# Performance work log

Measured on AMD Instinct MI355X. Metric: run time of the kernel, lower is better.

## Reference

```python
import jax, jax.numpy as jnp
import numpy as np

N, D, H, C = 50000, 128, 4, 16  # nodes, in_dim, heads, out per head
E, ED = 800000, 64              # edges, edge feature dim
NEG_SLOPE = 0.2


def setup_inputs() -> dict:
    key = jax.random.key(0)
    ks = jax.random.split(key, 10)
    x = jax.random.normal(ks[0], (N, D), dtype=jnp.float32)
    edge_index = jax.random.randint(ks[1], (2, E), 0, N, dtype=jnp.int64)
    edge_attr = jax.random.normal(ks[2], (E, ED), dtype=jnp.float32)
    s = 0.1
    W = jax.random.normal(ks[3], (H * C, D), dtype=jnp.float32) * s       # lin (no bias)
    W_edge = jax.random.normal(ks[4], (H * C, ED), dtype=jnp.float32) * s  # lin_edge (no bias)
    att_src = jax.random.normal(ks[5], (H, C), dtype=jnp.float32) * s
    att_dst = jax.random.normal(ks[6], (H, C), dtype=jnp.float32) * s
    att_edge = jax.random.normal(ks[7], (H, C), dtype=jnp.float32) * s
    bias = jnp.zeros((H * C,), dtype=jnp.float32)
    return dict(x=x, edge_index=edge_index, edge_attr=edge_attr, W=W,
                W_edge=W_edge, att_src=att_src, att_dst=att_dst,
                att_edge=att_edge, bias=bias)


def reference(x, edge_index, edge_attr, W, W_edge, att_src, att_dst, att_edge, bias):
    n = x.shape[0]
    src0, dst0 = edge_index[0], edge_index[1]

    # PyG GATConv default: add self-loops, self-loop edge_attr = per-dst mean of incoming edge_attr
    ones = jnp.ones((src0.shape[0],), dtype=edge_attr.dtype)
    cnt = jax.ops.segment_sum(ones, dst0, num_segments=n)                # [N]
    loop_attr = jax.ops.segment_sum(edge_attr, dst0, num_segments=n)
    loop_attr = loop_attr / jnp.maximum(cnt, 1.0)[:, None]               # [N, ED]
    ar = jnp.arange(n, dtype=src0.dtype)
    src = jnp.concatenate([src0, ar])
    dst = jnp.concatenate([dst0, ar])
    ea = jnp.concatenate([edge_attr, loop_attr], axis=0)                 # [E+N, ED]

    xh = (x @ W.T).reshape(n, H, C)                                      # [N, H, C]
    a_src = jnp.einsum('nhc,hc->nh', xh, att_src)                        # [N, H]
    a_dst = jnp.einsum('nhc,hc->nh', xh, att_dst)
    eh = (ea @ W_edge.T).reshape(-1, H, C)                               # [E+N, H, C]
    a_edge = jnp.einsum('ehc,hc->eh', eh, att_edge)                      # [E+N, H]

    alpha = a_src[src] + a_dst[dst] + a_edge                             # [E+N, H]
    alpha = jax.nn.leaky_relu(alpha, NEG_SLOPE)

    # softmax over edges grouped by destination node (PyG softmax)
    amax = jax.ops.segment_max(alpha, dst, num_segments=n)               # [N, H]
    alpha = jnp.exp(alpha - amax[dst])
    denom = jax.ops.segment_sum(alpha, dst, num_segments=n)
    alpha = alpha / (denom[dst] + 1e-16)

    # message = x_j * alpha, scatter-add to destination
    out = jax.ops.segment_sum(xh[src] * alpha[:, :, None], dst, num_segments=n)  # [N,H,C]
    return out.reshape(n, H * C) + bias
```

## Files before the change

kernel.cpp:

```cpp
#include <hip/hip_runtime.h>
#include <math.h>

#define N_NODES 50000
#define DIM     128
#define NHEAD   4
#define NCH     16
#define HC      64
#define NE      800000
#define EDIM    64
#define NEG     0.2f
#define MAXE    64

__device__ __forceinline__ float lrelu(float v) { return v > 0.f ? v : NEG * v; }

__global__ void k1_vedge(const float* __restrict__ W_edge, const float* __restrict__ att_edge,
                         float* __restrict__ v_edge) {
    int t = threadIdx.x;
    int h = t >> 6, d = t & 63;
    float acc = 0.f;
    #pragma unroll
    for (int c = 0; c < NCH; ++c)
        acc = fmaf(att_edge[h * NCH + c], W_edge[(h * NCH + c) * EDIM + d], acc);
    v_edge[h * 64 + d] = acc;
}

__global__ __launch_bounds__(256) void k2_xh(const float* __restrict__ x, const float* __restrict__ W,
                                             const float* __restrict__ att_src, const float* __restrict__ att_dst,
                                             float* __restrict__ xh, float* __restrict__ a_src,
                                             float* __restrict__ a_dst) {
    __shared__ float Wt[128 * 68];
    int t = threadIdx.x;
    for (int idx = t; idx < 64 * 128; idx += 256) {
        int col = idx >> 7, k = idx & 127;
        Wt[k * 68 + col] = W[idx];
    }
    __syncthreads();

    int h  = t & 3;
    int rp = t >> 2;
    int row0 = blockIdx.x * 128 + rp * 2;
    int r0 = min(row0, N_NODES - 1);
    int r1 = min(row0 + 1, N_NODES - 1);
    const float4* x0 = (const float4*)(x + (size_t)r0 * DIM);
    const float4* x1 = (const float4*)(x + (size_t)r1 * DIM);

    float acc0[16], acc1[16];
    #pragma unroll
    for (int c = 0; c < 16; ++c) { acc0[c] = 0.f; acc1[c] = 0.f; }

    for (int k4 = 0; k4 < 32; ++k4) {
        float4 xa = x0[k4];
        float4 xb = x1[k4];
        #pragma unroll
        for (int kk = 0; kk < 4; ++kk) {
            float va = (&xa.x)[kk];
            float vb = (&xb.x)[kk];
            const float* wr = &Wt[(k4 * 4 + kk) * 68 + h * 16];
            #pragma unroll
            for (int j = 0; j < 4; ++j) {
                float4 w = *(const float4*)(wr + 4 * j);
                acc0[4 * j + 0] = fmaf(va, w.x, acc0[4 * j + 0]);
                acc0[4 * j + 1] = fmaf(va, w.y, acc0[4 * j + 1]);
                acc0[4 * j + 2] = fmaf(va, w.z, acc0[4 * j + 2]);
                acc0[4 * j + 3] = fmaf(va, w.w, acc0[4 * j + 3]);
                acc1[4 * j + 0] = fmaf(vb, w.x, acc1[4 * j + 0]);
                acc1[4 * j + 1] = fmaf(vb, w.y, acc1[4 * j + 1]);
                acc1[4 * j + 2] = fmaf(vb, w.z, acc1[4 * j + 2]);
                acc1[4 * j + 3] = fmaf(vb, w.w, acc1[4 * j + 3]);
            }
        }
    }

    if (row0 < N_NODES) {
        float4* o = (float4*)(xh + (size_t)row0 * HC + h * 16);
        o[0] = make_float4(acc0[0], acc0[1], acc0[2], acc0[3]);
        o[1] = make_float4(acc0[4], acc0[5], acc0[6], acc0[7]);
        o[2] = make_float4(acc0[8], acc0[9], acc0[10], acc0[11]);
        o[3] = make_float4(acc0[12], acc0[13], acc0[14], acc0[15]);
        float ss = 0.f, sd = 0.f;
        #pragma unroll
        for (int c = 0; c < 16; ++c) {
            ss = fmaf(acc0[c], att_src[h * 16 + c], ss);
            sd = fmaf(acc0[c], att_dst[h * 16 + c], sd);
        }
        a_src[row0 * 4 + h] = ss;
        a_dst[row0 * 4 + h] = sd;
    }
    if (row0 + 1 < N_NODES) {
        float4* o = (float4*)(xh + (size_t)(row0 + 1) * HC + h * 16);
        o[0] = make_float4(acc1[0], acc1[1], acc1[2], acc1[3]);
        o[1] = make_float4(acc1[4], acc1[5], acc1[6], acc1[7]);
        o[2] = make_float4(acc1[8], acc1[9], acc1[10], acc1[11]);
        o[3] = make_float4(acc1[12], acc1[13], acc1[14], acc1[15]);
        float ss = 0.f, sd = 0.f;
        #pragma unroll
        for (int c = 0; c < 16; ++c) {
            ss = fmaf(acc1[c], att_src[h * 16 + c], ss);
            sd = fmaf(acc1[c], att_dst[h * 16 + c], sd);
        }
        a_src[(row0 + 1) * 4 + h] = ss;
        a_dst[(row0 + 1) * 4 + h] = sd;
    }
}

__global__ __launch_bounds__(256) void ka_deg(const int* __restrict__ ei, int* __restrict__ deg) {
    int e = blockIdx.x * 256 + threadIdx.x;
    if (e >= NE) return;
    atomicAdd(deg + ei[NE + e], 1);
}

__global__ void k4a_scan(const int* __restrict__ deg, int* __restrict__ tmp, int* __restrict__ bsums) {
    int t = threadIdx.x;
    int i = blockIdx.x * 256 + t;
    int v = (i < N_NODES) ? deg[i] : 0;
    int lane = t & 63, w = t >> 6;
    int xv = v;
    #pragma unroll
    for (int o = 1; o < 64; o <<= 1) {
        int y = __shfl_up(xv, o);
        if (lane >= o) xv += y;
    }
    __shared__ int wtot[4];
    if (lane == 63) wtot[w] = xv;
    __syncthreads();
    int add = 0;
    #pragma unroll
    for (int j = 0; j < 4; ++j)
        if (j < w) add += wtot[j];
    xv += add;
    if (i < N_NODES) tmp[i] = xv;
    if (t == 255) bsums[blockIdx.x] = xv;
}

__global__ void k4b_scan(int* __restrict__ bsums, int nb) {
    int t = threadIdx.x;
    int v = (t < nb) ? bsums[t] : 0;
    int lane = t & 63, w = t >> 6;
    int xv = v;
    #pragma unroll
    for (int o = 1; o < 64; o <<= 1) {
        int y = __shfl_up(xv, o);
        if (lane >= o) xv += y;
    }
    __shared__ int wtot[4];
    if (lane == 63) wtot[w] = xv;
    __syncthreads();
    int add = 0;
    #pragma unroll
    for (int j = 0; j < 4; ++j)
        if (j < w) add += wtot[j];
    xv += add;
    if (t < nb) bsums[t] = xv - v;
}

__global__ void k4c_finish(const int* __restrict__ tmp, const int* __restrict__ bsums,
                           const int* __restrict__ deg, int* __restrict__ rowptr,
                           int* __restrict__ cursor) {
    int i = blockIdx.x * 256 + threadIdx.x;
    if (i >= N_NODES) return;
    int incl = tmp[i] + bsums[i >> 8];
    rowptr[i + 1] = incl;
    cursor[i] = incl - deg[i];
    if (i == 0) rowptr[0] = 0;
}

__global__ __launch_bounds__(256) void kp_csr(const float* __restrict__ edge_attr,
                                              const int* __restrict__ ei,
                                              const float* __restrict__ v_edge,
                                              int* __restrict__ cursor,
                                              int* __restrict__ csr_src,
                                              float* __restrict__ csr_p) {
    int lane = threadIdx.x & 63;
    int q = lane & 15;
    float4 w0 = *(const float4*)(v_edge + 0 * 64 + q * 4);
    float4 w1 = *(const float4*)(v_edge + 1 * 64 + q * 4);
    float4 w2 = *(const float4*)(v_edge + 2 * 64 + q * 4);
    float4 w3 = *(const float4*)(v_edge + 3 * 64 + q * 4);

    int wave   = (blockIdx.x * 256 + threadIdx.x) >> 6;
    int nwaves = gridDim.x * 4;
    for (int g = wave; g < NE / 4; g += nwaves) {
        float4 v = *(const float4*)(edge_attr + (size_t)g * 256 + lane * 4);
        float p0 = fmaf(v.x, w0.x, fmaf(v.y, w0.y, fmaf(v.z, w0.z, v.w * w0.w)));
        float p1 = fmaf(v.x, w1.x, fmaf(v.y, w1.y, fmaf(v.z, w1.z, v.w * w1.w)));
        float p2 = fmaf(v.x, w2.x, fmaf(v.y, w2.y, fmaf(v.z, w2.z, v.w * w2.w)));
        float p3 = fmaf(v.x, w3.x, fmaf(v.y, w3.y, fmaf(v.z, w3.z, v.w * w3.w)));
        #pragma unroll
        for (int m = 1; m < 16; m <<= 1) {
            p0 += __shfl_xor(p0, m);
            p1 += __shfl_xor(p1, m);
            p2 += __shfl_xor(p2, m);
            p3 += __shfl_xor(p3, m);
        }
        if (q == 0) {
            int e = g * 4 + (lane >> 4);
            int src = ei[e];
            int dst = ei[NE + e];
            int pos = atomicAdd(cursor + dst, 1);
            csr_src[pos] = src;
            *(float4*)(csr_p + (size_t)pos * 4) = make_float4(p0, p1, p2, p3);
        }
    }
}

__global__ __launch_bounds__(256) void k6_agg(const int* __restrict__ rowptr,
                                              const int* __restrict__ csr_src,
                                              const float* __restrict__ csr_p,
                                              const float* __restrict__ xh,
                                              const float* __restrict__ a_src,
                                              const float* __restrict__ a_dst,
                                              const float* __restrict__ bias,
                                              float* __restrict__ out) {
    __shared__ __align__(16) float s_w[4][MAXE][4];
    __shared__ int s_src[4][MAXE];
    int wid  = threadIdx.x >> 6;
    int lane = threadIdx.x & 63;
    int n = blockIdx.x * 4 + wid;
    int start = rowptr[n], end = rowptr[n + 1];
    int degn = end - start;
    int m = min(degn, MAXE);

    for (int i = lane; i < m; i += 64) {
        s_src[wid][i] = csr_src[start + i];
        *(float4*)&s_w[wid][i][0] = *(const float4*)(csr_p + (size_t)(start + i) * 4);
    }
    __syncthreads();

    int h = lane & 3;
    float adh = a_dst[n * 4 + h];
    float sw = 0.f, sp = 0.f;
    for (int i = lane >> 2; i < m; i += 16) {
        int s   = s_src[wid][i];
        float p = s_w[wid][i][h];
        float w = __expf(lrelu(a_src[(size_t)s * 4 + h] + adh + p));
        s_w[wid][i][h] = w;
        sw += w;
        sp += p;
    }
    for (int i = MAXE + (lane >> 2); i < degn; i += 16) {
        int s = csr_src[start + i];
        float p = csr_p[(size_t)(start + i) * 4 + h];
        sw += __expf(lrelu(a_src[(size_t)s * 4 + h] + adh + p));
        sp += p;
    }
    sw += __shfl_xor(sw, 4);  sp += __shfl_xor(sp, 4);
    sw += __shfl_xor(sw, 8);  sp += __shfl_xor(sp, 8);
    sw += __shfl_xor(sw, 16); sp += __shfl_xor(sp, 16);
    sw += __shfl_xor(sw, 32); sp += __shfl_xor(sp, 32);

    float al    = sp / fmaxf((float)degn, 1.f);
    float wself = __expf(lrelu(a_src[n * 4 + h] + adh + al));
    float denom = sw + wself + 1e-16f;
    __syncthreads();

    int h2 = lane >> 4;
    float d2   = __shfl(denom, h2);
    float ws2  = __shfl(wself, h2);
    float adh2 = __shfl(adh, h2);
    float acc = ws2 * xh[(size_t)n * HC + lane];

    int i = 0;
    for (; i + 4 <= m; i += 4) {
        int s0 = s_src[wid][i], s1 = s_src[wid][i + 1];
        int s2 = s_src[wid][i + 2], s3 = s_src[wid][i + 3];
        float w0 = s_w[wid][i][h2],     w1 = s_w[wid][i + 1][h2];
        float w2 = s_w[wid][i + 2][h2], w3 = s_w[wid][i + 3][h2];
        float x0 = xh[(size_t)s0 * HC + lane];
        float x1 = xh[(size_t)s1 * HC + lane];
        float x2 = xh[(size_t)s2 * HC + lane];
        float x3 = xh[(size_t)s3 * HC + lane];
        acc = fmaf(w0, x0, acc);
        acc = fmaf(w1, x1, acc);
        acc = fmaf(w2, x2, acc);
        acc = fmaf(w3, x3, acc);
    }
    for (; i < m; ++i) {
        int s = s_src[wid][i];
        acc = fmaf(s_w[wid][i][h2], xh[(size_t)s * HC + lane], acc);
    }
    for (int j = MAXE; j < degn; ++j) {
        int s = csr_src[start + j];
        float p = csr_p[(size_t)(start + j) * 4 + h2];
        float w = __expf(lrelu(a_src[(size_t)s * 4 + h2] + adh2 + p));
        acc = fmaf(w, xh[(size_t)s * HC + lane], acc);
    }
    out[(size_t)n * HC + lane] = acc / d2 + bias[lane];
}

extern "C" void kernel_launch(void* const* d_in, const int* in_sizes, int n_in,
                              void* d_out, int out_size, void* d_ws, size_t ws_size,
                              hipStream_t stream) {
    const float* x         = (const float*)d_in[0];
    const int*   ei        = (const int*)d_in[1];
    const float* edge_attr = (const float*)d_in[2];
    const float* W         = (const float*)d_in[3];
    const float* W_edge    = (const float*)d_in[4];
    const float* att_src   = (const float*)d_in[5];
    const float* att_dst   = (const float*)d_in[6];
    const float* att_edge  = (const float*)d_in[7];
    const float* bias      = (const float*)d_in[8];
    float* out = (float*)d_out;

    char* ws = (char*)d_ws;
    size_t off = 0;
    float* v_edge    = (float*)(ws + off); off += 1024;
    float* xh        = (float*)(ws + off); off += (size_t)N_NODES * HC * 4;
    float* a_src     = (float*)(ws + off); off += (size_t)N_NODES * 4 * 4;
    float* a_dst     = (float*)(ws + off); off += (size_t)N_NODES * 4 * 4;
    int*   deg       = (int*)(ws + off);   off += (size_t)N_NODES * 4;
    int*   tmp       = (int*)(ws + off);   off += (size_t)N_NODES * 4;
    int*   bsums     = (int*)(ws + off);   off += 1024;
    int*   rowptr    = (int*)(ws + off);   off += (size_t)(N_NODES + 4) * 4;
    int*   cursor    = (int*)(ws + off);   off += (size_t)N_NODES * 4;
    int*   csr_src   = (int*)(ws + off);   off += (size_t)NE * 4;
    float* csr_p     = (float*)(ws + off); off += (size_t)NE * 4 * 4;

    hipMemsetAsync(deg, 0, (size_t)N_NODES * 4, stream);

    k1_vedge<<<1, 256, 0, stream>>>(W_edge, att_edge, v_edge);
    k2_xh<<<(N_NODES + 127) / 128, 256, 0, stream>>>(x, W, att_src, att_dst, xh, a_src, a_dst);
    ka_deg<<<(NE + 255) / 256, 256, 0, stream>>>(ei, deg);
    int nb = (N_NODES + 255) / 256;
    k4a_scan<<<nb, 256, 0, stream>>>(deg, tmp, bsums);
    k4b_scan<<<1, 256, 0, stream>>>(bsums, nb);
    k4c_finish<<<nb, 256, 0, stream>>>(tmp, bsums, deg, rowptr, cursor);
    kp_csr<<<1024, 256, 0, stream>>>(edge_attr, ei, v_edge, cursor, csr_src, csr_p);
    k6_agg<<<N_NODES / 4, 256, 0, stream>>>(rowptr, csr_src, csr_p, xh,
                                            a_src, a_dst, bias, out);
}
```

Baseline: 466.3 us.

## Build CSR via atomic ranks and permutation instead of scattering edge data

The degree-count kernel now records each edge's atomic rank, and a separate permutation kernel places edge ids at rowptr[dst]+rank. This removes the cursor atomics in the edge-projection pass. Edge logits are written in original edge order, and the aggregation kernel gathers source ids and logits indirectly through the permutation. The intent is to drop the second atomic pass and the scattered writes of 20-byte records, at the cost of an extra kernel and indirect random gathers in the aggregation.

```diff
diff --git a/kernel.cpp b/kernel.cpp
--- a/kernel.cpp
+++ b/kernel.cpp
@@ -103,10 +103,11 @@
     }
 }
 
-__global__ __launch_bounds__(256) void ka_deg(const int* __restrict__ ei, int* __restrict__ deg) {
+__global__ __launch_bounds__(256) void ka_deg(const int* __restrict__ ei, int* __restrict__ deg,
+                                              int* __restrict__ rank) {
     int e = blockIdx.x * 256 + threadIdx.x;
     if (e >= NE) return;
-    atomicAdd(deg + ei[NE + e], 1);
+    rank[e] = atomicAdd(deg + ei[NE + e], 1);
 }
 
 __global__ void k4a_scan(const int* __restrict__ deg, int* __restrict__ tmp, int* __restrict__ bsums) {
@@ -154,22 +155,17 @@
 }
 
 __global__ void k4c_finish(const int* __restrict__ tmp, const int* __restrict__ bsums,
-                           const int* __restrict__ deg, int* __restrict__ rowptr,
-                           int* __restrict__ cursor) {
+                           int* __restrict__ rowptr) {
     int i = blockIdx.x * 256 + threadIdx.x;
     if (i >= N_NODES) return;
     int incl = tmp[i] + bsums[i >> 8];
     rowptr[i + 1] = incl;
-    cursor[i] = incl - deg[i];
     if (i == 0) rowptr[0] = 0;
 }
 
-__global__ __launch_bounds__(256) void kp_csr(const float* __restrict__ edge_attr,
-                                              const int* __restrict__ ei,
-                                              const float* __restrict__ v_edge,
-                                              int* __restrict__ cursor,
-                                              int* __restrict__ csr_src,
-                                              float* __restrict__ csr_p) {
+__global__ __launch_bounds__(256) void kp_compute(const float* __restrict__ edge_attr,
+                                                  const float* __restrict__ v_edge,
+                                                  float* __restrict__ p_tmp) {
     int lane = threadIdx.x & 63;
     int q = lane & 15;
     float4 w0 = *(const float4*)(v_edge + 0 * 64 + q * 4);
@@ -194,18 +190,25 @@
         }
         if (q == 0) {
             int e = g * 4 + (lane >> 4);
-            int src = ei[e];
-            int dst = ei[NE + e];
-            int pos = atomicAdd(cursor + dst, 1);
-            csr_src[pos] = src;
-            *(float4*)(csr_p + (size_t)pos * 4) = make_float4(p0, p1, p2, p3);
-        }
-    }
+            *(float4*)(p_tmp + (size_t)e * 4) = make_float4(p0, p1, p2, p3);
+        }
+    }
+}
+
+__global__ __launch_bounds__(256) void kp_perm(const int* __restrict__ ei,
+                                               const int* __restrict__ rank,
+                                               const int* __restrict__ rowptr,
+                                               int* __restrict__ perm) {
+    int e = blockIdx.x * 256 + threadIdx.x;
+    if (e >= NE) return;
+    int dst = ei[NE + e];
+    perm[rowptr[dst] + rank[e]] = e;
 }
 
 __global__ __launch_bounds__(256) void k6_agg(const int* __restrict__ rowptr,
-                                              const int* __restrict__ csr_src,
-                                              const float* __restrict__ csr_p,
+                                              const int* __restrict__ perm,
+                                              const int* __restrict__ ei,
+                                              const float* __restrict__ p_tmp,
                                               const float* __restrict__ xh,
                                               const float* __restrict__ a_src,
                                               const float* __restrict__ a_dst,
@@ -221,8 +224,9 @@
     int m = min(degn, MAXE);
 
     for (int i = lane; i < m; i += 64) {
-        s_src[wid][i] = csr_src[start + i];
-        *(float4*)&s_w[wid][i][0] = *(const float4*)(csr_p + (size_t)(start + i) * 4);
+        int e = perm[start + i];
+        s_src[wid][i] = ei[e];
+        *(float4*)&s_w[wid][i][0] = *(const float4*)(p_tmp + (size_t)e * 4);
     }
     __syncthreads();
 
@@ -238,8 +242,9 @@
         sp += p;
     }
     for (int i = MAXE + (lane >> 2); i < degn; i += 16) {
-        int s = csr_src[start + i];
-        float p = csr_p[(size_t)(start + i) * 4 + h];
+        int e = perm[start + i];
+        int s = ei[e];
+        float p = p_tmp[(size_t)e * 4 + h];
         sw += __expf(lrelu(a_src[(size_t)s * 4 + h] + adh + p));
         sp += p;
     }
@@ -279,8 +284,9 @@
         acc = fmaf(s_w[wid][i][h2], xh[(size_t)s * HC + lane], acc);
     }
     for (int j = MAXE; j < degn; ++j) {
-        int s = csr_src[start + j];
-        float p = csr_p[(size_t)(start + j) * 4 + h2];
+        int e = perm[start + j];
+        int s = ei[e];
+        float p = p_tmp[(size_t)e * 4 + h2];
         float w = __expf(lrelu(a_src[(size_t)s * 4 + h2] + adh2 + p));
         acc = fmaf(w, xh[(size_t)s * HC + lane], acc);
     }
@@ -311,20 +317,21 @@
     int*   tmp       = (int*)(ws + off);   off += (size_t)N_NODES * 4;
     int*   bsums     = (int*)(ws + off);   off += 1024;
     int*   rowptr    = (int*)(ws + off);   off += (size_t)(N_NODES + 4) * 4;
-    int*   cursor    = (int*)(ws + off);   off += (size_t)N_NODES * 4;
-    int*   csr_src   = (int*)(ws + off);   off += (size_t)NE * 4;
-    float* csr_p     = (float*)(ws + off); off += (size_t)NE * 4 * 4;
+    int*   rank      = (int*)(ws + off);   off += (size_t)NE * 4;
+    int*   perm      = (int*)(ws + off);   off += (size_t)NE * 4;
+    float* p_tmp     = (float*)(ws + off); off += (size_t)NE * 4 * 4;
 
     hipMemsetAsync(deg, 0, (size_t)N_NODES * 4, stream);
 
     k1_vedge<<<1, 256, 0, stream>>>(W_edge, att_edge, v_edge);
     k2_xh<<<(N_NODES + 127) / 128, 256, 0, stream>>>(x, W, att_src, att_dst, xh, a_src, a_dst);
-    ka_deg<<<(NE + 255) / 256, 256, 0, stream>>>(ei, deg);
+    ka_deg<<<(NE + 255) / 256, 256, 0, stream>>>(ei, deg, rank);
     int nb = (N_NODES + 255) / 256;
     k4a_scan<<<nb, 256, 0, stream>>>(deg, tmp, bsums);
     k4b_scan<<<1, 256, 0, stream>>>(bsums, nb);
-    k4c_finish<<<nb, 256, 0, stream>>>(tmp, bsums, deg, rowptr, cursor);
-    kp_csr<<<1024, 256, 0, stream>>>(edge_attr, ei, v_edge, cursor, csr_src, csr_p);
-    k6_agg<<<N_NODES / 4, 256, 0, stream>>>(rowptr, csr_src, csr_p, xh,
+    k4c_finish<<<nb, 256, 0, stream>>>(tmp, bsums, rowptr);
+    kp_compute<<<2048, 256, 0, stream>>>(edge_attr, v_edge, p_tmp);
+    kp_perm<<<(NE + 255) / 256, 256, 0, stream>>>(ei, rank, rowptr, perm);
+    k6_agg<<<N_NODES / 4, 256, 0, stream>>>(rowptr, perm, ei, p_tmp, xh,
                                             a_src, a_dst, bias, out);
 }
```

Result: faster. 449.2 us (-3.7%).
